# Kernel tuning notes

Hardware: AMD Instinct MI355X
Metric: run time of the kernel (lower is better)

The kernel has to match this reference:

```python
import jax, jax.numpy as jnp
import numpy as np

K = 15          # k_point_level
EPS = 1e-5      # BatchNorm eps
NEG = 0.2       # LeakyReLU slope


def _lrelu(y):
    return jnp.where(y > 0, y, NEG * y)


def _knn_idx(x, k):
    # x: [N, C, P] -> idx [N, P, k] of nearest points (incl. self) by -||xi-xj||^2 topk
    inner = -2.0 * jnp.einsum('ncp,ncq->npq', x, x)
    xx = jnp.sum(x * x, axis=1)                      # [N, P]
    pd = -xx[:, :, None] - inner - xx[:, None, :]    # [N, P, P]
    return jax.lax.top_k(pd, k)[1]


def _edge_feature(x, k):
    # x: [N, C, P] -> [N, P, k, 2C] = concat(neigh - center, center)
    N = x.shape[0]
    idx = _knn_idx(x, k)                             # [N, P, k]
    xt = jnp.transpose(x, (0, 2, 1))                 # [N, P, C]
    neigh = xt[jnp.arange(N)[:, None, None], idx]    # [N, P, k, C]
    center = jnp.broadcast_to(xt[:, :, None, :], neigh.shape)
    return jnp.concatenate([neigh - center, center], axis=-1)


def _edge_block(x, W, gamma, beta, k):
    # EdgeConv: gather -> 1x1 conv -> BN (batch stats) -> LeakyReLU -> max over k
    f = _edge_feature(x, k)                          # [N, P, k, 2C]
    y = jnp.einsum('npkc,oc->npko', f, W)
    m = jnp.mean(y, axis=(0, 1, 2))
    v = jnp.var(y, axis=(0, 1, 2))
    y = (y - m) * jax.lax.rsqrt(v + EPS) * gamma + beta
    y = jnp.max(_lrelu(y), axis=2)                   # [N, P, O]
    return jnp.transpose(y, (0, 2, 1))               # [N, O, P]


def _forward(x, W1, g1, b1, W2, g2, b2, W3, g3, b3, W4, g4, b4,
             W5, g5, b5, Wl1, g6, b6, Wl2, bl2, g7, b7, Wl3, bl3):
    x1 = _edge_block(x, W1, g1, b1, K)               # [N, 64, P]
    x2 = _edge_block(x1, W2, g2, b2, K)              # [N, 64, P]
    x3 = _edge_block(x2, W3, g3, b3, K)              # [N, 128, P]
    x4 = _edge_block(x3, W4, g4, b4, K)              # [N, 256, P]
    xc = jnp.concatenate([x1, x2, x3, x4], axis=1)   # [N, 512, P]
    y = jnp.einsum('ncp,oc->npo', xc, W5)            # [N, P, emb]
    m = jnp.mean(y, axis=(0, 1)); v = jnp.var(y, axis=(0, 1))
    y = _lrelu((y - m) * jax.lax.rsqrt(v + EPS) * g5 + b5)
    h = jnp.concatenate([jnp.max(y, axis=1), jnp.mean(y, axis=1)], axis=1)  # [N, 2*emb]
    h = h @ Wl1.T
    m = jnp.mean(h, axis=0); v = jnp.var(h, axis=0)
    h = _lrelu((h - m) * jax.lax.rsqrt(v + EPS) * g6 + b6)
    h = h @ Wl2.T + bl2
    m = jnp.mean(h, axis=0); v = jnp.var(h, axis=0)
    h = _lrelu((h - m) * jax.lax.rsqrt(v + EPS) * g7 + b7)
    logits = h @ Wl3.T + bl3
    return jax.nn.log_softmax(logits, axis=1)


def setup_inputs() -> dict:
    key = jax.random.key(0)
    ks = iter(jax.random.split(key, 16))
    N, P, EMB, NC = 2048, 32, 1024, 800

    def w(k, o, i):
        return jax.random.normal(k, (o, i), jnp.float32) / np.sqrt(i)

    d = {
        'x': jax.random.normal(next(ks), (N, 3, P), jnp.float32),
        'info_point_set': jnp.zeros((1,), jnp.float32),
        'W1': w(next(ks), 64, 6),   'g1': jnp.ones(64),  'b1': jnp.zeros(64),
        'W2': w(next(ks), 64, 128), 'g2': jnp.ones(64),  'b2': jnp.zeros(64),
        'W3': w(next(ks), 128, 128),'g3': jnp.ones(128), 'b3': jnp.zeros(128),
        'W4': w(next(ks), 256, 256),'g4': jnp.ones(256), 'b4': jnp.zeros(256),
        'W5': w(next(ks), EMB, 512),'g5': jnp.ones(EMB), 'b5': jnp.zeros(EMB),
        'Wl1': w(next(ks), 512, 2 * EMB), 'g6': jnp.ones(512), 'b6': jnp.zeros(512),
        'Wl2': w(next(ks), 256, 512), 'bl2': jnp.zeros(256),
        'g7': jnp.ones(256), 'b7': jnp.zeros(256),
        'Wl3': w(next(ks), NC, 256), 'bl3': jnp.zeros(NC),
    }
    return d


def reference(x, info_point_set, W1, g1, b1, W2, g2, b2, W3, g3, b3,
              W4, g4, b4, W5, g5, b5, Wl1, g6, b6, Wl2, bl2, g7, b7, Wl3, bl3):
    # info_point_set unused: args.k + args.k_global == 0 path (dynamic KNN graph).
    return _forward(x, W1, g1, b1, W2, g2, b2, W3, g3, b3, W4, g4, b4,
                    W5, g5, b5, Wl1, g6, b6, Wl2, bl2, g7, b7, Wl3, bl3)
```

## Files before the change

### kernel.cpp

```cpp
#include <hip/hip_runtime.h>
#include <hip/hip_bf16.h>
#include <cstdint>
#include <cstddef>

#define NPTS 2048
#define P 32
#define KNN_K 15
#define LRELU_NEG 0.2f
#define BN_EPS 1e-5f

__device__ __forceinline__ float lrelu(float x) { return x > 0.f ? x : LRELU_NEG * x; }

__device__ __forceinline__ unsigned short f2bf(float x) {
    union { float f; unsigned u; } uu; uu.f = x;
    unsigned r = uu.u + 0x7fffu + ((uu.u >> 16) & 1u);
    return (unsigned short)(r >> 16);
}
__device__ __forceinline__ float bf2f(unsigned short b) {
    union { unsigned u; float f; } uu; uu.u = ((unsigned)b) << 16;
    return uu.f;
}

typedef short bf16x8 __attribute__((ext_vector_type(8)));
typedef float f32x4  __attribute__((ext_vector_type(4)));

template<int C>
__global__ __launch_bounds__(64) void knn_kernel(const float* __restrict__ xin, int cloudStride,
                                                 unsigned char* __restrict__ idx)
{
    const int n = blockIdx.x, t = threadIdx.x;
    __shared__ float xs[C][P];
    __shared__ float xx[P];
    __shared__ float pd[P][P + 1];
    const float* xp = xin + (size_t)n * cloudStride;
    for (int i = t; i < C * P; i += 64) xs[i / P][i % P] = xp[i];
    __syncthreads();
    if (t < P) { float s = 0.f; for (int c = 0; c < C; ++c) { float v = xs[c][t]; s = fmaf(v, v, s); } xx[t] = s; }
    __syncthreads();
    for (int i = t; i < P * P; i += 64) {
        int p = i >> 5, q = i & 31;
        float d = 0.f;
        for (int c = 0; c < C; ++c) d = fmaf(xs[c][p], xs[c][q], d);
        pd[p][q] = 2.f * d - xx[p] - xx[q];
    }
    __syncthreads();
    if (t < P) {
        for (int j = 0; j < KNN_K; ++j) {
            float best = -INFINITY; int bq = 0;
            for (int q = 0; q < P; ++q) { float v = pd[t][q]; if (v > best) { best = v; bq = q; } }
            idx[(size_t)n * (P * KNN_K) + t * KNN_K + j] = (unsigned char)bq;
            pd[t][bq] = -INFINITY;
        }
    }
}

__global__ __launch_bounds__(256) void build_wcat_kernel(const float* __restrict__ W, float* __restrict__ wt,
                                                         int C, int O, int NCHUNK)
{
    int i = blockIdx.x * 256 + threadIdx.x;
    int tot = C * 2 * O;
    if (i >= tot) return;
    int c = i / (2 * O), col = i % (2 * O);
    int O2C = 2 * O / NCHUNK, OC = O / NCHUNK;
    int chunk = col / O2C, cl = col % O2C;
    float v;
    if (cl < OC) { int o = chunk * OC + cl; v = W[(size_t)o * 2 * C + c]; }
    else { int o = chunk * OC + cl - OC; v = W[(size_t)o * 2 * C + C + c] - W[(size_t)o * 2 * C + c]; }
    wt[i] = v;
}

__global__ __launch_bounds__(256) void pack_wcat_kernel(const float* __restrict__ wt,
                                                        unsigned short* __restrict__ wpk,
                                                        int C, int TOTC)
{
    int NTT = TOTC / 16;
    int total = C * TOTC;
    int i = blockIdx.x * 256 + threadIdx.x;
    if (i >= total) return;
    int j = i & 7, lane = (i >> 3) & 63;
    int rest = i >> 9;
    int ntg = rest % NTT, kb = rest / NTT;
    int k = kb * 32 + (lane >> 4) * 8 + j;
    int col = ntg * 16 + (lane & 15);
    float f = wt[(size_t)k * TOTC + col];
    unsigned short hi = f2bf(f);
    unsigned short lo = f2bf(f - bf2f(hi));
    size_t base = (size_t)rest * 1024 + (size_t)lane * 8 + j;
    wpk[base] = hi;
    wpk[base + 512] = lo;
}

template<int C, int O, int NCHUNK, bool OUT>
__global__ __launch_bounds__(256) void edge_pass_kernel(
    const float* __restrict__ xin, int cloudStride,
    const float* __restrict__ wt,
    const unsigned char* __restrict__ idx,
    const float* __restrict__ st,
    float* __restrict__ xcout,
    float* __restrict__ partS, float* __restrict__ partQ)
{
    constexpr int TOTC = 2 * O;
    constexpr int O2C = TOTC / NCHUNK;
    constexpr int OC  = O / NCHUNK;
    constexpr int TPC = (O2C >= 256) ? 1 : (256 / O2C);
    constexpr int CPT = (O2C > 256) ? (O2C / 256) : 1;
    constexpr int PP  = P / TPC;
    constexpr int TPO = 256 / OC;
    constexpr int PPo = P / TPO;
    const int n = blockIdx.x, t = threadIdx.x;

    __shared__ float xs[C][P];
    __shared__ float gh[P * O2C];
    __shared__ unsigned char idl[P * KNN_K];
    __shared__ float red[2][256];

    const float* xp = xin + (size_t)n * cloudStride;
    for (int i = t; i < C * P; i += 256) xs[i / P][i % P] = xp[i];
    for (int i = t; i < P * KNN_K; i += 256) idl[i] = idx[(size_t)n * (P * KNN_K) + i];

    const int col = (O2C >= 256) ? t : (t % O2C);
    const int p0  = ((O2C >= 256) ? 0 : (t / O2C)) * PP;
    const int o   = t % OC;
    const int p0c = (t / OC) * PPo;

    for (int chunk = 0; chunk < NCHUNK; ++chunk) {
        __syncthreads();
        {
            float acc[CPT][PP];
            #pragma unroll
            for (int j = 0; j < CPT; ++j)
                #pragma unroll
                for (int p = 0; p < PP; ++p) acc[j][p] = 0.f;
            for (int c = 0; c < C; ++c) {
                float w[CPT];
                #pragma unroll
                for (int j = 0; j < CPT; ++j) w[j] = wt[(size_t)c * TOTC + chunk * O2C + col + j * 256];
                #pragma unroll
                for (int p = 0; p < PP; ++p) {
                    float xv = xs[c][p0 + p];
                    #pragma unroll
                    for (int j = 0; j < CPT; ++j) acc[j][p] = fmaf(w[j], xv, acc[j][p]);
                }
            }
            #pragma unroll
            for (int j = 0; j < CPT; ++j)
                #pragma unroll
                for (int p = 0; p < PP; ++p) gh[(p0 + p) * O2C + col + j * 256] = acc[j][p];
        }
        __syncthreads();

        if constexpr (!OUT) {
            float ssum = 0.f, ssq = 0.f;
            #pragma unroll
            for (int p = 0; p < PPo; ++p) {
                const int pp = p0c + p;
                const float g = gh[pp * O2C + OC + o];
                #pragma unroll
                for (int k = 0; k < KNN_K; ++k) {
                    const int q = idl[pp * KNN_K + k];
                    float yv = gh[q * O2C + o] + g;
                    ssum += yv; ssq += yv * yv;
                }
            }
            red[0][t] = ssum; red[1][t] = ssq;
            __syncthreads();
            if (t < OC) {
                float S = 0.f, Q = 0.f;
                #pragma unroll
                for (int j = 0; j < TPO; ++j) { S += red[0][t + j * OC]; Q += red[1][t + j * OC]; }
                partS[(size_t)(chunk * OC + t) * 2048 + n] = S;
                partQ[(size_t)(chunk * OC + t) * 2048 + n] = Q;
            }
        } else {
            const float s = st[chunk * OC + o], sh = st[1024 + chunk * OC + o];
            float rbuf[PPo];
            #pragma unroll
            for (int p = 0; p < PPo; ++p) {
                const int pp = p0c + p;
                const float g = gh[pp * O2C + OC + o];
                float mx = -INFINITY, mn = INFINITY;
                #pragma unroll
                for (int k = 0; k < KNN_K; ++k) {
                    const int q = idl[pp * KNN_K + k];
                    float yv = gh[q * O2C + o] + g;
                    mx = fmaxf(mx, yv); mn = fminf(mn, yv);
                }
                rbuf[p] = lrelu(fmaf(s, (s >= 0.f ? mx : mn), sh));
            }
            __syncthreads();
            #pragma unroll
            for (int p = 0; p < PPo; ++p) gh[o * (P + 1) + p0c + p] = rbuf[p];
            __syncthreads();
            for (int i = t; i < OC * P; i += 256)
                xcout[(size_t)n * (512 * P) + chunk * OC * P + i] = gh[(i / P) * (P + 1) + (i % P)];
        }
    }
}

template<int C, int O, bool OUT>
__global__ __launch_bounds__(256) void edge_mfma_kernel(
    const float* __restrict__ xin, int cloudStride,
    const unsigned short* __restrict__ wpk,
    const unsigned char* __restrict__ idx,
    const float* __restrict__ st,
    float* __restrict__ xcout,
    float* __restrict__ partS, float* __restrict__ partQ)
{
    constexpr int TOTC  = 2 * O;
    constexpr int O2C   = (TOTC > 256) ? 256 : TOTC;
    constexpr int NCHUNK= TOTC / O2C;
    constexpr int OC    = O2C / 2;
    constexpr int NTW   = O2C / 64;
    constexpr int KB    = C / 32;
    constexpr int NTT   = TOTC / 16;
    constexpr int AS    = C + 8;
    constexpr int GHS   = O2C + 4;
    constexpr int TPO   = 256 / OC;
    constexpr int PPo   = P / TPO;

    const int n = blockIdx.x, t = threadIdx.x;
    const int w = t >> 6, l = t & 63;
    const int lg = l >> 4, lm = l & 15;

    __shared__ unsigned short Ah[P * AS];
    __shared__ unsigned short Al[P * AS];
    __shared__ float gh[P * GHS];
    __shared__ unsigned char idl[P * KNN_K];

    const float* xp = xin + (size_t)n * cloudStride;
    for (int i = t; i < C * P; i += 256) {
        int c = i / P, p = i % P;
        float v = xp[i];
        unsigned short hi = f2bf(v);
        Ah[p * AS + c] = hi;
        Al[p * AS + c] = f2bf(v - bf2f(hi));
    }
    for (int i = t; i < P * KNN_K; i += 256) idl[i] = idx[(size_t)n * (P * KNN_K) + i];
    __syncthreads();

    const int o = t % OC;
    const int p0c = (t / OC) * PPo;

    for (int chunk = 0; chunk < NCHUNK; ++chunk) {
        f32x4 acc[2][NTW];
        #pragma unroll
        for (int mt = 0; mt < 2; ++mt)
            #pragma unroll
            for (int nt = 0; nt < NTW; ++nt) acc[mt][nt] = (f32x4)0.f;

        #pragma unroll
        for (int kb = 0; kb < KB; ++kb) {
            bf16x8 a_h[2], a_l[2];
            #pragma unroll
            for (int mt = 0; mt < 2; ++mt) {
                int row = mt * 16 + lm;
                a_h[mt] = *(const bf16x8*)&Ah[row * AS + kb * 32 + lg * 8];
                a_l[mt] = *(const bf16x8*)&Al[row * AS + kb * 32 + lg * 8];
            }
            #pragma unroll
            for (int nt = 0; nt < NTW; ++nt) {
                int ntg = chunk * (O2C / 16) + w * NTW + nt;
                const unsigned short* bp = wpk + (size_t)(kb * NTT + ntg) * 1024 + (size_t)l * 8;
                bf16x8 Bh = *(const bf16x8*)bp;
                bf16x8 Bl = *(const bf16x8*)(bp + 512);
                #pragma unroll
                for (int mt = 0; mt < 2; ++mt) {
                    acc[mt][nt] = __builtin_amdgcn_mfma_f32_16x16x32_bf16(a_h[mt], Bl, acc[mt][nt], 0, 0, 0);
                    acc[mt][nt] = __builtin_amdgcn_mfma_f32_16x16x32_bf16(a_l[mt], Bh, acc[mt][nt], 0, 0, 0);
                    acc[mt][nt] = __builtin_amdgcn_mfma_f32_16x16x32_bf16(a_h[mt], Bh, acc[mt][nt], 0, 0, 0);
                }
            }
        }
        __syncthreads();
        #pragma unroll
        for (int mt = 0; mt < 2; ++mt)
            #pragma unroll
            for (int nt = 0; nt < NTW; ++nt) {
                int colb = (w * NTW + nt) * 16 + lm;
                #pragma unroll
                for (int r = 0; r < 4; ++r)
                    gh[(mt * 16 + lg * 4 + r) * GHS + colb] = acc[mt][nt][r];
            }
        __syncthreads();

        if constexpr (!OUT) {
            float ssum = 0.f, ssq = 0.f;
            #pragma unroll
            for (int p = 0; p < PPo; ++p) {
                const int pp = p0c + p;
                const float g = gh[pp * GHS + OC + o];
                #pragma unroll
                for (int k = 0; k < KNN_K; ++k) {
                    const int q = idl[pp * KNN_K + k];
                    float yv = gh[q * GHS + o] + g;
                    ssum += yv; ssq += yv * yv;
                }
            }
            __syncthreads();
            gh[t] = ssum; gh[256 + t] = ssq;
            __syncthreads();
            if (t < OC) {
                float S = 0.f, Q = 0.f;
                #pragma unroll
                for (int j = 0; j < TPO; ++j) { S += gh[t + j * OC]; Q += gh[256 + t + j * OC]; }
                partS[(size_t)(chunk * OC + t) * 2048 + n] = S;
                partQ[(size_t)(chunk * OC + t) * 2048 + n] = Q;
            }
        } else {
            const float s = st[chunk * OC + o], sh = st[1024 + chunk * OC + o];
            float rbuf[PPo];
            #pragma unroll
            for (int p = 0; p < PPo; ++p) {
                const int pp = p0c + p;
                const float g = gh[pp * GHS + OC + o];
                float mx = -INFINITY, mn = INFINITY;
                #pragma unroll
                for (int k = 0; k < KNN_K; ++k) {
                    const int q = idl[pp * KNN_K + k];
                    float yv = gh[q * GHS + o] + g;
                    mx = fmaxf(mx, yv); mn = fminf(mn, yv);
                }
                rbuf[p] = lrelu(fmaf(s, (s >= 0.f ? mx : mn), sh));
            }
            __syncthreads();
            #pragma unroll
            for (int p = 0; p < PPo; ++p) gh[o * (P + 1) + p0c + p] = rbuf[p];
            __syncthreads();
            for (int i = t; i < OC * P; i += 256)
                xcout[(size_t)n * (512 * P) + chunk * OC * P + i] = gh[(i / P) * (P + 1) + (i % P)];
        }
    }
}

__global__ __launch_bounds__(256) void reduce_stats_kernel(const float* __restrict__ partS,
                                                           const float* __restrict__ partQ,
                                                           const float* __restrict__ gamma,
                                                           const float* __restrict__ beta,
                                                           float* __restrict__ st, int nparts, float inv_count)
{
    const int o = blockIdx.x, t = threadIdx.x;
    __shared__ float rs[256], rq[256];
    float S = 0.f, Q = 0.f;
    for (int i = t; i < nparts; i += 256) { S += partS[(size_t)o * 2048 + i]; Q += partQ[(size_t)o * 2048 + i]; }
    rs[t] = S; rq[t] = Q; __syncthreads();
    for (int w = 128; w > 0; w >>= 1) { if (t < w) { rs[t] += rs[t + w]; rq[t] += rq[t + w]; } __syncthreads(); }
    if (t == 0) {
        float m = rs[0] * inv_count;
        float v = fmaxf(rq[0] * inv_count - m * m, 0.f);
        float s = gamma[o] * rsqrtf(v + BN_EPS);
        st[o] = s;
        st[1024 + o] = fmaf(-m, s, beta[o]);
    }
}

__global__ __launch_bounds__(256) void pack_w5_kernel(const float* __restrict__ W5, unsigned short* __restrict__ wp)
{
    int i = blockIdx.x * 256 + threadIdx.x;
    if (i >= (1 << 19)) return;
    int j = i & 7, lane = (i >> 3) & 63, nt = (i >> 9) & 63, kb = i >> 15;
    int c = kb * 32 + (lane >> 4) * 8 + j;
    int o = nt * 16 + (lane & 15);
    float f = W5[(size_t)o * 512 + c];
    unsigned short hi = f2bf(f);
    unsigned short lo = f2bf(f - bf2f(hi));
    size_t base = (size_t)(kb * 64 + nt) * 2 * 512 + (size_t)lane * 8 + j;
    wp[base] = hi;
    wp[base + 512] = lo;
}

__global__ __launch_bounds__(512) void conv5_store_kernel(
    const float* xc, const unsigned short* __restrict__ wpack,
    unsigned short* y5,
    float* __restrict__ partS, float* __restrict__ partQ)
{
    const int b = blockIdx.x;
    const int t = threadIdx.x;
    const int w = t >> 6, l = t & 63;
    const int lg = l >> 4, lm = l & 15;

    __shared__ unsigned short Ah[2][64][40];
    __shared__ unsigned short Al[2][64][40];

    f32x4 acc[4][8];
    #pragma unroll
    for (int mt = 0; mt < 4; ++mt)
        #pragma unroll
        for (int nt = 0; nt < 8; ++nt) acc[mt][nt] = (f32x4)0.f;

    const float* xbase = xc + (size_t)(b * 2) * (512 * P);

    const int sp4    = t & 7;
    const int schalf = (t >> 3) & 15;
    const int scloud = (t >> 7) & 1;
    const bool sact  = t < 256;

    auto stage = [&](int kb, int buf) {
        if (sact) {
            const float* src = xbase + (size_t)scloud * (512 * P)
                             + (size_t)(kb * 32 + 2 * schalf) * P + sp4 * 4;
            const float4 v0 = *(const float4*)src;
            const float4 v1 = *(const float4*)(src + P);
            const int r0 = scloud * 32 + sp4 * 4;
            #pragma unroll
            for (int e = 0; e < 4; ++e) {
                float a0 = (&v0.x)[e], a1 = (&v1.x)[e];
                unsigned short h0 = f2bf(a0), h1 = f2bf(a1);
                unsigned short l0 = f2bf(a0 - bf2f(h0)), l1 = f2bf(a1 - bf2f(h1));
                *(unsigned*)&Ah[buf][r0 + e][2 * schalf] = (unsigned)h0 | ((unsigned)h1 << 16);
                *(unsigned*)&Al[buf][r0 + e][2 * schalf] = (unsigned)l0 | ((unsigned)l1 << 16);
            }
        }
    };

    stage(0, 0);
    int cur = 0;
    for (int kb = 0; kb < 16; ++kb) {
        __syncthreads();
        if (kb + 1 < 16) stage(kb + 1, cur ^ 1);

        bf16x8 a_h[4], a_l[4];
        #pragma unroll
        for (int mt = 0; mt < 4; ++mt) {
            int row = mt * 16 + lm;
            a_h[mt] = *(const bf16x8*)&Ah[cur][row][lg * 8];
            a_l[mt] = *(const bf16x8*)&Al[cur][row][lg * 8];
        }
        #pragma unroll
        for (int nt = 0; nt < 8; ++nt) {
            const int ntg = w * 8 + nt;
            const unsigned short* bp = wpack + (size_t)(kb * 64 + ntg) * 2 * 512 + (size_t)l * 8;
            bf16x8 Bh = *(const bf16x8*)bp;
            bf16x8 Bl = *(const bf16x8*)(bp + 512);
            #pragma unroll
            for (int mt = 0; mt < 4; ++mt) {
                acc[mt][nt] = __builtin_amdgcn_mfma_f32_16x16x32_bf16(a_h[mt], Bl, acc[mt][nt], 0, 0, 0);
                acc[mt][nt] = __builtin_amdgcn_mfma_f32_16x16x32_bf16(a_l[mt], Bh, acc[mt][nt], 0, 0, 0);
                acc[mt][nt] = __builtin_amdgcn_mfma_f32_16x16x32_bf16(a_h[mt], Bh, acc[mt][nt], 0, 0, 0);
            }
        }
        cur ^= 1;
    }
    __syncthreads();

    #pragma unroll
    for (int nt = 0; nt < 8; ++nt) {
        float s = 0.f, q = 0.f;
        #pragma unroll
        for (int mt = 0; mt < 4; ++mt)
            #pragma unroll
            for (int r = 0; r < 4; ++r) { float v = acc[mt][nt][r]; s += v; q = fmaf(v, v, q); }
        s += __shfl_xor(s, 16); q += __shfl_xor(q, 16);
        s += __shfl_xor(s, 32); q += __shfl_xor(q, 32);
        if (l < 16) {
            int o = w * 128 + nt * 16 + lm;
            partS[(size_t)o * 2048 + b] = s;
            partQ[(size_t)o * 2048 + b] = q;
        }
        #pragma unroll
        for (int mt = 0; mt < 4; ++mt) {
            unsigned p0 = (unsigned)f2bf(acc[mt][nt][0]) | ((unsigned)f2bf(acc[mt][nt][1]) << 16);
            unsigned p1 = (unsigned)f2bf(acc[mt][nt][2]) | ((unsigned)f2bf(acc[mt][nt][3]) << 16);
            size_t off = ((((size_t)b * 8 + w) * 8 + nt) * 4 + mt) * 64 + l;
            ((uint2*)y5)[off] = make_uint2(p0, p1);
        }
    }
}

__global__ __launch_bounds__(512) void conv5_finish_kernel(
    const unsigned short* __restrict__ y5, const float* __restrict__ st, float* __restrict__ h)
{
    const int b = blockIdx.x, t = threadIdx.x;
    const int w = t >> 6, l = t & 63, lm = l & 15;
    #pragma unroll
    for (int nt = 0; nt < 8; ++nt) {
        const int o = w * 128 + nt * 16 + lm;
        const float sc = st[o], sh = st[1024 + o];
        #pragma unroll
        for (int cloud = 0; cloud < 2; ++cloud) {
            float mx = -INFINITY, sm = 0.f;
            #pragma unroll
            for (int half = 0; half < 2; ++half) {
                const int mt = cloud * 2 + half;
                uint2 pk = ((const uint2*)y5)[((((size_t)b * 8 + w) * 8 + nt) * 4 + mt) * 64 + l];
                #pragma unroll
                for (int r = 0; r < 4; ++r) {
                    unsigned word = (r < 2) ? pk.x : pk.y;
                    unsigned short bits = (unsigned short)((r & 1) ? (word >> 16) : (word & 0xffff));
                    float v = lrelu(fmaf(sc, bf2f(bits), sh));
                    mx = fmaxf(mx, v); sm += v;
                }
            }
            mx = fmaxf(mx, __shfl_xor(mx, 16)); sm += __shfl_xor(sm, 16);
            mx = fmaxf(mx, __shfl_xor(mx, 32)); sm += __shfl_xor(sm, 32);
            if (l < 16) {
                const int n = b * 2 + cloud;
                h[(size_t)n * 2048 + o] = mx;
                h[(size_t)n * 2048 + 1024 + o] = sm * (1.f / 32.f);
            }
        }
    }
}

__global__ __launch_bounds__(256) void gemm_nt(const float* __restrict__ A, const float* __restrict__ B,
                                               const float* __restrict__ bias, float* __restrict__ Cc,
                                               int M, int Nn, int Kk)
{
    __shared__ float As[16][64];
    __shared__ float Bs[16][64];
    const int t = threadIdx.x;
    const int m0 = blockIdx.y * 64;
    const int o0 = blockIdx.x * 64;
    const int lm = t % 64;
    const int lk4 = (t / 64) * 4;
    const int tx = t % 16, ty = t / 16;
    float acc[4][4] = {};
    for (int k0 = 0; k0 < Kk; k0 += 16) {
        float4 av4 = *(const float4*)(A + (size_t)(m0 + lm) * Kk + k0 + lk4);
        float4 bv4 = make_float4(0.f, 0.f, 0.f, 0.f);
        if (o0 + lm < Nn) bv4 = *(const float4*)(B + (size_t)(o0 + lm) * Kk + k0 + lk4);
        __syncthreads();
        As[lk4 + 0][lm] = av4.x; As[lk4 + 1][lm] = av4.y; As[lk4 + 2][lm] = av4.z; As[lk4 + 3][lm] = av4.w;
        Bs[lk4 + 0][lm] = bv4.x; Bs[lk4 + 1][lm] = bv4.y; Bs[lk4 + 2][lm] = bv4.z; Bs[lk4 + 3][lm] = bv4.w;
        __syncthreads();
        #pragma unroll
        for (int kk = 0; kk < 16; ++kk) {
            float a[4], b[4];
            *(float4*)a = *(const float4*)&As[kk][ty * 4];
            *(float4*)b = *(const float4*)&Bs[kk][tx * 4];
            #pragma unroll
            for (int i = 0; i < 4; ++i)
                #pragma unroll
                for (int j = 0; j < 4; ++j) acc[i][j] = fmaf(a[i], b[j], acc[i][j]);
        }
    }
    #pragma unroll
    for (int i = 0; i < 4; ++i) {
        int m = m0 + ty * 4 + i;
        #pragma unroll
        for (int j = 0; j < 4; ++j) {
            int o = o0 + tx * 4 + j;
            if (o < Nn) Cc[(size_t)m * Nn + o] = acc[i][j] + (bias ? bias[o] : 0.f);
        }
    }
    (void)M;
}

template<int NCPT>
__global__ __launch_bounds__(256) void colstats_kernel(const float* __restrict__ A, int NC,
                                                       float* __restrict__ partS, float* __restrict__ partQ)
{
    const int b = blockIdx.x, t = threadIdx.x;
    float S[NCPT], Q[NCPT];
    #pragma unroll
    for (int j = 0; j < NCPT; ++j) { S[j] = 0.f; Q[j] = 0.f; }
    for (int r = 0; r < 32; ++r) {
        const float* row = A + (size_t)(b * 32 + r) * NC;
        #pragma unroll
        for (int j = 0; j < NCPT; ++j) { float v = row[t + j * 256]; S[j] += v; Q[j] += v * v; }
    }
    #pragma unroll
    for (int j = 0; j < NCPT; ++j) {
        int o = t + j * 256;
        partS[(size_t)o * 2048 + b] = S[j];
        partQ[(size_t)o * 2048 + b] = Q[j];
    }
}

__global__ __launch_bounds__(256) void bnact_kernel(const float* __restrict__ in, const float* __restrict__ st,
                                                    float* __restrict__ out, int NC, int total)
{
    int i = blockIdx.x * 256 + threadIdx.x;
    if (i < total) {
        int o = i % NC;
        out[i] = lrelu(fmaf(st[o], in[i], st[1024 + o]));
    }
}

__global__ __launch_bounds__(256) void logsoftmax_kernel(float* __restrict__ out)
{
    const int n = blockIdx.x, t = threadIdx.x;
    float* row = out + (size_t)n * 800;
    __shared__ float red[256];
    float v[4];
    float mx = -INFINITY;
    #pragma unroll
    for (int j = 0; j < 4; ++j) {
        int i = t + j * 256;
        v[j] = (i < 800) ? row[i] : -INFINITY;
        mx = fmaxf(mx, v[j]);
    }
    red[t] = mx; __syncthreads();
    for (int w = 128; w > 0; w >>= 1) { if (t < w) red[t] = fmaxf(red[t], red[t + w]); __syncthreads(); }
    const float m = red[0]; __syncthreads();
    float s = 0.f;
    #pragma unroll
    for (int j = 0; j < 4; ++j) { int i = t + j * 256; if (i < 800) s += expf(v[j] - m); }
    red[t] = s; __syncthreads();
    for (int w = 128; w > 0; w >>= 1) { if (t < w) red[t] += red[t + w]; __syncthreads(); }
    const float lg = m + logf(red[0]);
    #pragma unroll
    for (int j = 0; j < 4; ++j) { int i = t + j * 256; if (i < 800) row[i] = v[j] - lg; }
}

extern "C" void kernel_launch(void* const* d_in, const int* in_sizes, int n_in,
                              void* d_out, int out_size, void* d_ws, size_t ws_size,
                              hipStream_t stream)
{
    (void)in_sizes; (void)n_in; (void)out_size; (void)ws_size;
    const float* x   = (const float*)d_in[0];
    const float* W1  = (const float*)d_in[2];
    const float* g1  = (const float*)d_in[3];
    const float* b1  = (const float*)d_in[4];
    const float* W2  = (const float*)d_in[5];
    const float* g2  = (const float*)d_in[6];
    const float* b2  = (const float*)d_in[7];
    const float* W3  = (const float*)d_in[8];
    const float* g3  = (const float*)d_in[9];
    const float* b3  = (const float*)d_in[10];
    const float* W4  = (const float*)d_in[11];
    const float* g4  = (const float*)d_in[12];
    const float* b4  = (const float*)d_in[13];
    const float* W5  = (const float*)d_in[14];
    const float* g5  = (const float*)d_in[15];
    const float* b5  = (const float*)d_in[16];
    const float* Wl1 = (const float*)d_in[17];
    const float* g6  = (const float*)d_in[18];
    const float* b6  = (const float*)d_in[19];
    const float* Wl2 = (const float*)d_in[20];
    const float* bl2 = (const float*)d_in[21];
    const float* g7  = (const float*)d_in[22];
    const float* b7  = (const float*)d_in[23];
    const float* Wl3 = (const float*)d_in[24];
    const float* bl3 = (const float*)d_in[25];

    char* ws = (char*)d_ws;
    size_t off = 0;
    auto alloc = [&](size_t bytes) -> void* {
        void* p = ws + off; off += (bytes + 255) & ~(size_t)255; return p;
    };
    float*          xc    = (float*)alloc((size_t)NPTS * 512 * P * 4);
    unsigned char*  idx   = (unsigned char*)alloc((size_t)NPTS * P * KNN_K);
    float*          partS = (float*)alloc((size_t)1024 * 2048 * 4);
    float*          partQ = (float*)alloc((size_t)1024 * 2048 * 4);
    float*          st    = (float*)alloc(2048 * 4);
    float*          wt    = (float*)alloc((size_t)512 * 1024 * 4);
    unsigned short* wpk   = (unsigned short*)alloc((size_t)128 * 512 * 2 * 2);
    float*          h     = (float*)alloc((size_t)2048 * 2048 * 4);
    float*          h1p   = (float*)alloc((size_t)2048 * 512 * 4);
    unsigned short* y5 = (unsigned short*)xc;
    float* h1  = h;
    float* h2p = h + 1048576;
    float* h2  = h + 1572864;

    const float inv_edge = 1.f / (float)(NPTS * P * KNN_K);

    knn_kernel<3><<<NPTS, 64, 0, stream>>>(x, 3 * P, idx);
    build_wcat_kernel<<<(3 * 128 + 255) / 256, 256, 0, stream>>>(W1, wt, 3, 64, 1);
    edge_pass_kernel<3, 64, 1, false><<<NPTS, 256, 0, stream>>>(x, 3 * P, wt, idx, nullptr, nullptr, partS, partQ);
    reduce_stats_kernel<<<64, 256, 0, stream>>>(partS, partQ, g1, b1, st, 2048, inv_edge);
    edge_pass_kernel<3, 64, 1, true><<<NPTS, 256, 0, stream>>>(x, 3 * P, wt, idx, st, xc + 0 * P, nullptr, nullptr);

    knn_kernel<64><<<NPTS, 64, 0, stream>>>(xc, 512 * P, idx);
    build_wcat_kernel<<<(64 * 128 + 255) / 256, 256, 0, stream>>>(W2, wt, 64, 64, 1);
    pack_wcat_kernel<<<(64 * 128 + 255) / 256, 256, 0, stream>>>(wt, wpk, 64, 128);
    edge_mfma_kernel<64, 64, false><<<NPTS, 256, 0, stream>>>(xc, 512 * P, wpk, idx, nullptr, nullptr, partS, partQ);
    reduce_stats_kernel<<<64, 256, 0, stream>>>(partS, partQ, g2, b2, st, 2048, inv_edge);
    edge_mfma_kernel<64, 64, true><<<NPTS, 256, 0, stream>>>(xc, 512 * P, wpk, idx, st, xc + 64 * P, nullptr, nullptr);

    knn_kernel<64><<<NPTS, 64, 0, stream>>>(xc + 64 * P, 512 * P, idx);
    build_wcat_kernel<<<(64 * 256 + 255) / 256, 256, 0, stream>>>(W3, wt, 64, 128, 1);
    pack_wcat_kernel<<<(64 * 256 + 255) / 256, 256, 0, stream>>>(wt, wpk, 64, 256);
    edge_mfma_kernel<64, 128, false><<<NPTS, 256, 0, stream>>>(xc + 64 * P, 512 * P, wpk, idx, nullptr, nullptr, partS, partQ);
    reduce_stats_kernel<<<128, 256, 0, stream>>>(partS, partQ, g3, b3, st, 2048, inv_edge);
    edge_mfma_kernel<64, 128, true><<<NPTS, 256, 0, stream>>>(xc + 64 * P, 512 * P, wpk, idx, st, xc + 128 * P, nullptr, nullptr);

    knn_kernel<128><<<NPTS, 64, 0, stream>>>(xc + 128 * P, 512 * P, idx);
    build_wcat_kernel<<<(128 * 512 + 255) / 256, 256, 0, stream>>>(W4, wt, 128, 256, 2);
    pack_wcat_kernel<<<(128 * 512 + 255) / 256, 256, 0, stream>>>(wt, wpk, 128, 512);
    edge_mfma_kernel<128, 256, false><<<NPTS, 256, 0, stream>>>(xc + 128 * P, 512 * P, wpk, idx, nullptr, nullptr, partS, partQ);
    reduce_stats_kernel<<<256, 256, 0, stream>>>(partS, partQ, g4, b4, st, 2048, inv_edge);
    edge_mfma_kernel<128, 256, true><<<NPTS, 256, 0, stream>>>(xc + 128 * P, 512 * P, wpk, idx, st, xc + 256 * P, nullptr, nullptr);

    pack_w5_kernel<<<2048, 256, 0, stream>>>(W5, (unsigned short*)wt);
    conv5_store_kernel<<<1024, 512, 0, stream>>>(xc, (const unsigned short*)wt, y5, partS, partQ);
    reduce_stats_kernel<<<1024, 256, 0, stream>>>(partS, partQ, g5, b5, st, 1024, 1.f / 65536.f);
    conv5_finish_kernel<<<1024, 512, 0, stream>>>(y5, st, h);

    gemm_nt<<<dim3(512 / 64, 2048 / 64), 256, 0, stream>>>(h, Wl1, nullptr, h1p, 2048, 512, 2048);
    colstats_kernel<2><<<64, 256, 0, stream>>>(h1p, 512, partS, partQ);
    reduce_stats_kernel<<<512, 256, 0, stream>>>(partS, partQ, g6, b6, st, 64, 1.f / 2048.f);
    bnact_kernel<<<(2048 * 512 + 255) / 256, 256, 0, stream>>>(h1p, st, h1, 512, 2048 * 512);

    gemm_nt<<<dim3(256 / 64, 2048 / 64), 256, 0, stream>>>(h1, Wl2, bl2, h2p, 2048, 256, 512);
    colstats_kernel<1><<<64, 256, 0, stream>>>(h2p, 256, partS, partQ);
    reduce_stats_kernel<<<256, 256, 0, stream>>>(partS, partQ, g7, b7, st, 64, 1.f / 2048.f);
    bnact_kernel<<<(2048 * 256 + 255) / 256, 256, 0, stream>>>(h2p, st, h2, 256, 2048 * 256);

    gemm_nt<<<dim3((800 + 63) / 64, 2048 / 64), 256, 0, stream>>>(h2, Wl3, bl3, (float*)d_out, 2048, 800, 256);
    logsoftmax_kernel<<<NPTS, 256, 0, stream>>>((float*)d_out);
}
```

Measured before the change: 946.7 us.

## Move FC head GEMMs to split-bf16 MFMA with fused BN stats and input activation

Replaces the scalar fp32 tiled GEMM for the three classifier linear layers with an MFMA kernel. It uses a hi/lo bf16 split (three MFMAs per tile) to keep near-fp32 accuracy, with weights pre-packed by a new pack kernel. Column statistics are now accumulated in the GEMM epilogue, and the BN+LeakyReLU of the previous layer is applied while staging the input. This drops the separate colstats and bnact passes. Edge-conv weight packing also merges the build and pack kernels into one. In exchange there are extra bf16 conversion steps, and the split-bf16 arithmetic may differ slightly from plain fp32.

```diff
diff --git a/kernel.cpp b/kernel.cpp
--- a/kernel.cpp
+++ b/kernel.cpp
@@ -69,25 +69,41 @@
     wt[i] = v;
 }
 
-__global__ __launch_bounds__(256) void pack_wcat_kernel(const float* __restrict__ wt,
+__global__ __launch_bounds__(256) void pack_wcat_direct(const float* __restrict__ W,
                                                         unsigned short* __restrict__ wpk,
-                                                        int C, int TOTC)
-{
-    int NTT = TOTC / 16;
-    int total = C * TOTC;
+                                                        int C, int O, int NCHUNK)
+{
+    const int TOTC = 2 * O, NTT = TOTC / 16;
+    const int O2C = TOTC / NCHUNK, OC = O / NCHUNK;
     int i = blockIdx.x * 256 + threadIdx.x;
-    if (i >= total) return;
-    int j = i & 7, lane = (i >> 3) & 63;
-    int rest = i >> 9;
+    if (i >= C * TOTC) return;
+    int j = i & 7, lane = (i >> 3) & 63, rest = i >> 9;
     int ntg = rest % NTT, kb = rest / NTT;
     int k = kb * 32 + (lane >> 4) * 8 + j;
     int col = ntg * 16 + (lane & 15);
-    float f = wt[(size_t)k * TOTC + col];
-    unsigned short hi = f2bf(f);
-    unsigned short lo = f2bf(f - bf2f(hi));
-    size_t base = (size_t)rest * 1024 + (size_t)lane * 8 + j;
-    wpk[base] = hi;
-    wpk[base + 512] = lo;
+    int chunk = col / O2C, cl = col % O2C;
+    float v;
+    if (cl < OC) { int o = chunk * OC + cl; v = W[(size_t)o * 2 * C + k]; }
+    else         { int o = chunk * OC + cl - OC; v = W[(size_t)o * 2 * C + C + k] - W[(size_t)o * 2 * C + k]; }
+    unsigned short hi = f2bf(v);
+    wpk[(size_t)rest * 1024 + lane * 8 + j] = hi;
+    wpk[(size_t)rest * 1024 + 512 + lane * 8 + j] = f2bf(v - bf2f(hi));
+}
+
+__global__ __launch_bounds__(256) void pack_wfc_kernel(const float* __restrict__ W,
+                                                       unsigned short* __restrict__ wpk,
+                                                       int Kk, int Nn, int NTT)
+{
+    int i = blockIdx.x * 256 + threadIdx.x;
+    if (i >= NTT * 16 * Kk) return;
+    int j = i & 7, lane = (i >> 3) & 63, rest = i >> 9;
+    int ntg = rest % NTT, kb = rest / NTT;
+    int k = kb * 32 + (lane >> 4) * 8 + j;
+    int col = ntg * 16 + (lane & 15);
+    float v = (col < Nn) ? W[(size_t)col * Kk + k] : 0.f;
+    unsigned short hi = f2bf(v);
+    wpk[(size_t)rest * 1024 + lane * 8 + j] = hi;
+    wpk[(size_t)rest * 1024 + 512 + lane * 8 + j] = f2bf(v - bf2f(hi));
 }
 
 template<int C, int O, int NCHUNK, bool OUT>
@@ -501,78 +517,102 @@
     }
 }
 
-__global__ __launch_bounds__(256) void gemm_nt(const float* __restrict__ A, const float* __restrict__ B,
-                                               const float* __restrict__ bias, float* __restrict__ Cc,
-                                               int M, int Nn, int Kk)
-{
-    __shared__ float As[16][64];
-    __shared__ float Bs[16][64];
+template<bool BNIN, bool STATS>
+__global__ __launch_bounds__(256) void gemm_mfma_nt(
+    const float* __restrict__ A, const unsigned short* __restrict__ wpk,
+    const float* __restrict__ stbn, const float* __restrict__ bias,
+    float* __restrict__ Cc, float* __restrict__ partS, float* __restrict__ partQ,
+    int Nn, int NTT, int Kk)
+{
+    const int o0 = blockIdx.x * 64;
+    const int m0 = blockIdx.y * 64;
     const int t = threadIdx.x;
-    const int m0 = blockIdx.y * 64;
-    const int o0 = blockIdx.x * 64;
-    const int lm = t % 64;
-    const int lk4 = (t / 64) * 4;
-    const int tx = t % 16, ty = t / 16;
-    float acc[4][4] = {};
-    for (int k0 = 0; k0 < Kk; k0 += 16) {
-        float4 av4 = *(const float4*)(A + (size_t)(m0 + lm) * Kk + k0 + lk4);
-        float4 bv4 = make_float4(0.f, 0.f, 0.f, 0.f);
-        if (o0 + lm < Nn) bv4 = *(const float4*)(B + (size_t)(o0 + lm) * Kk + k0 + lk4);
+    const int w = t >> 6, l = t & 63;
+    const int lg = l >> 4, lm = l & 15;
+
+    __shared__ unsigned short Ah[2][64][40];
+    __shared__ unsigned short Al[2][64][40];
+
+    f32x4 acc[4];
+    #pragma unroll
+    for (int mt = 0; mt < 4; ++mt) acc[mt] = (f32x4)0.f;
+
+    const int srow = t >> 3;
+    const int sk4  = (t & 7) * 4;
+
+    auto stage = [&](int kb, int buf) {
+        const float* src = A + (size_t)(m0 + srow) * Kk + kb * 32 + sk4;
+        float4 v0 = *(const float4*)src;
+        float4 v1 = *(const float4*)(src + (size_t)32 * Kk);
+        if (BNIN) {
+            const float4 s4 = *(const float4*)(stbn + kb * 32 + sk4);
+            const float4 t4 = *(const float4*)(stbn + 1024 + kb * 32 + sk4);
+            #pragma unroll
+            for (int e = 0; e < 4; ++e) {
+                (&v0.x)[e] = lrelu(fmaf((&s4.x)[e], (&v0.x)[e], (&t4.x)[e]));
+                (&v1.x)[e] = lrelu(fmaf((&s4.x)[e], (&v1.x)[e], (&t4.x)[e]));
+            }
+        }
+        #pragma unroll
+        for (int e = 0; e < 4; e += 2) {
+            float a0 = (&v0.x)[e], a1 = (&v0.x)[e + 1];
+            unsigned short h0 = f2bf(a0), h1 = f2bf(a1);
+            *(unsigned*)&Ah[buf][srow][sk4 + e] = (unsigned)h0 | ((unsigned)h1 << 16);
+            *(unsigned*)&Al[buf][srow][sk4 + e] =
+                (unsigned)f2bf(a0 - bf2f(h0)) | ((unsigned)f2bf(a1 - bf2f(h1)) << 16);
+            float b0 = (&v1.x)[e], b1 = (&v1.x)[e + 1];
+            unsigned short g0 = f2bf(b0), g1 = f2bf(b1);
+            *(unsigned*)&Ah[buf][srow + 32][sk4 + e] = (unsigned)g0 | ((unsigned)g1 << 16);
+            *(unsigned*)&Al[buf][srow + 32][sk4 + e] =
+                (unsigned)f2bf(b0 - bf2f(g0)) | ((unsigned)f2bf(b1 - bf2f(g1)) << 16);
+        }
+    };
+
+    const int KB = Kk >> 5;
+    stage(0, 0);
+    int cur = 0;
+    const int ntg = blockIdx.x * 4 + w;
+    for (int kb = 0; kb < KB; ++kb) {
         __syncthreads();
-        As[lk4 + 0][lm] = av4.x; As[lk4 + 1][lm] = av4.y; As[lk4 + 2][lm] = av4.z; As[lk4 + 3][lm] = av4.w;
-        Bs[lk4 + 0][lm] = bv4.x; Bs[lk4 + 1][lm] = bv4.y; Bs[lk4 + 2][lm] = bv4.z; Bs[lk4 + 3][lm] = bv4.w;
-        __syncthreads();
-        #pragma unroll
-        for (int kk = 0; kk < 16; ++kk) {
-            float a[4], b[4];
-            *(float4*)a = *(const float4*)&As[kk][ty * 4];
-            *(float4*)b = *(const float4*)&Bs[kk][tx * 4];
-            #pragma unroll
-            for (int i = 0; i < 4; ++i)
-                #pragma unroll
-                for (int j = 0; j < 4; ++j) acc[i][j] = fmaf(a[i], b[j], acc[i][j]);
-        }
-    }
+        if (kb + 1 < KB) stage(kb + 1, cur ^ 1);
+        bf16x8 a_h[4], a_l[4];
+        #pragma unroll
+        for (int mt = 0; mt < 4; ++mt) {
+            a_h[mt] = *(const bf16x8*)&Ah[cur][mt * 16 + lm][lg * 8];
+            a_l[mt] = *(const bf16x8*)&Al[cur][mt * 16 + lm][lg * 8];
+        }
+        const unsigned short* bp = wpk + ((size_t)kb * NTT + ntg) * 1024 + (size_t)l * 8;
+        bf16x8 Bh = *(const bf16x8*)bp;
+        bf16x8 Bl = *(const bf16x8*)(bp + 512);
+        #pragma unroll
+        for (int mt = 0; mt < 4; ++mt) {
+            acc[mt] = __builtin_amdgcn_mfma_f32_16x16x32_bf16(a_h[mt], Bl, acc[mt], 0, 0, 0);
+            acc[mt] = __builtin_amdgcn_mfma_f32_16x16x32_bf16(a_l[mt], Bh, acc[mt], 0, 0, 0);
+            acc[mt] = __builtin_amdgcn_mfma_f32_16x16x32_bf16(a_h[mt], Bh, acc[mt], 0, 0, 0);
+        }
+        cur ^= 1;
+    }
+
+    const int col = o0 + w * 16 + lm;
+    const bool cok = col < Nn;
+    const float bv = (bias != nullptr && cok) ? bias[col] : 0.f;
+    float s = 0.f, q = 0.f;
     #pragma unroll
-    for (int i = 0; i < 4; ++i) {
-        int m = m0 + ty * 4 + i;
-        #pragma unroll
-        for (int j = 0; j < 4; ++j) {
-            int o = o0 + tx * 4 + j;
-            if (o < Nn) Cc[(size_t)m * Nn + o] = acc[i][j] + (bias ? bias[o] : 0.f);
-        }
-    }
-    (void)M;
-}
-
-template<int NCPT>
-__global__ __launch_bounds__(256) void colstats_kernel(const float* __restrict__ A, int NC,
-                                                       float* __restrict__ partS, float* __restrict__ partQ)
-{
-    const int b = blockIdx.x, t = threadIdx.x;
-    float S[NCPT], Q[NCPT];
-    #pragma unroll
-    for (int j = 0; j < NCPT; ++j) { S[j] = 0.f; Q[j] = 0.f; }
-    for (int r = 0; r < 32; ++r) {
-        const float* row = A + (size_t)(b * 32 + r) * NC;
-        #pragma unroll
-        for (int j = 0; j < NCPT; ++j) { float v = row[t + j * 256]; S[j] += v; Q[j] += v * v; }
-    }
-    #pragma unroll
-    for (int j = 0; j < NCPT; ++j) {
-        int o = t + j * 256;
-        partS[(size_t)o * 2048 + b] = S[j];
-        partQ[(size_t)o * 2048 + b] = Q[j];
-    }
-}
-
-__global__ __launch_bounds__(256) void bnact_kernel(const float* __restrict__ in, const float* __restrict__ st,
-                                                    float* __restrict__ out, int NC, int total)
-{
-    int i = blockIdx.x * 256 + threadIdx.x;
-    if (i < total) {
-        int o = i % NC;
-        out[i] = lrelu(fmaf(st[o], in[i], st[1024 + o]));
+    for (int mt = 0; mt < 4; ++mt) {
+        #pragma unroll
+        for (int r = 0; r < 4; ++r) {
+            float v = acc[mt][r] + bv;
+            if (STATS) { s += v; q = fmaf(v, v, q); }
+            if (cok) Cc[(size_t)(m0 + mt * 16 + lg * 4 + r) * Nn + col] = v;
+        }
+    }
+    if (STATS) {
+        s += __shfl_xor(s, 16); q += __shfl_xor(q, 16);
+        s += __shfl_xor(s, 32); q += __shfl_xor(q, 32);
+        if (l < 16 && cok) {
+            partS[(size_t)col * 2048 + blockIdx.y] = s;
+            partQ[(size_t)col * 2048 + blockIdx.y] = q;
+        }
     }
 }
 
@@ -645,12 +685,11 @@
     float*          st    = (float*)alloc(2048 * 4);
     float*          wt    = (float*)alloc((size_t)512 * 1024 * 4);
     unsigned short* wpk   = (unsigned short*)alloc((size_t)128 * 512 * 2 * 2);
+    unsigned short* fcpk  = (unsigned short*)alloc((size_t)512 * 2048 * 2 * 2);
     float*          h     = (float*)alloc((size_t)2048 * 2048 * 4);
     float*          h1p   = (float*)alloc((size_t)2048 * 512 * 4);
     unsigned short* y5 = (unsigned short*)xc;
-    float* h1  = h;
     float* h2p = h + 1048576;
-    float* h2  = h + 1572864;
 
     const float inv_edge = 1.f / (float)(NPTS * P * KNN_K);
 
@@ -661,22 +700,19 @@
     edge_pass_kernel<3, 64, 1, true><<<NPTS, 256, 0, stream>>>(x, 3 * P, wt, idx, st, xc + 0 * P, nullptr, nullptr);
 
     knn_kernel<64><<<NPTS, 64, 0, stream>>>(xc, 512 * P, idx);
-    build_wcat_kernel<<<(64 * 128 + 255) / 256, 256, 0, stream>>>(W2, wt, 64, 64, 1);
-    pack_wcat_kernel<<<(64 * 128 + 255) / 256, 256, 0, stream>>>(wt, wpk, 64, 128);
+    pack_wcat_direct<<<(64 * 128 + 255) / 256, 256, 0, stream>>>(W2, wpk, 64, 64, 1);
     edge_mfma_kernel<64, 64, false><<<NPTS, 256, 0, stream>>>(xc, 512 * P, wpk, idx, nullptr, nullptr, partS, partQ);
     reduce_stats_kernel<<<64, 256, 0, stream>>>(partS, partQ, g2, b2, st, 2048, inv_edge);
     edge_mfma_kernel<64, 64, true><<<NPTS, 256, 0, stream>>>(xc, 512 * P, wpk, idx, st, xc + 64 * P, nullptr, nullptr);
 
     knn_kernel<64><<<NPTS, 64, 0, stream>>>(xc + 64 * P, 512 * P, idx);
-    build_wcat_kernel<<<(64 * 256 + 255) / 256, 256, 0, stream>>>(W3, wt, 64, 128, 1);
-    pack_wcat_kernel<<<(64 * 256 + 255) / 256, 256, 0, stream>>>(wt, wpk, 64, 256);
+    pack_wcat_direct<<<(64 * 256 + 255) / 256, 256, 0, stream>>>(W3, wpk, 64, 128, 1);
     edge_mfma_kernel<64, 128, false><<<NPTS, 256, 0, stream>>>(xc + 64 * P, 512 * P, wpk, idx, nullptr, nullptr, partS, partQ);
     reduce_stats_kernel<<<128, 256, 0, stream>>>(partS, partQ, g3, b3, st, 2048, inv_edge);
     edge_mfma_kernel<64, 128, true><<<NPTS, 256, 0, stream>>>(xc + 64 * P, 512 * P, wpk, idx, st, xc + 128 * P, nullptr, nullptr);
 
     knn_kernel<128><<<NPTS, 64, 0, stream>>>(xc + 128 * P, 512 * P, idx);
-    build_wcat_kernel<<<(128 * 512 + 255) / 256, 256, 0, stream>>>(W4, wt, 128, 256, 2);
-    pack_wcat_kernel<<<(128 * 512 + 255) / 256, 256, 0, stream>>>(wt, wpk, 128, 512);
+    pack_wcat_direct<<<(128 * 512 + 255) / 256, 256, 0, stream>>>(W4, wpk, 128, 256, 2);
     edge_mfma_kernel<128, 256, false><<<NPTS, 256, 0, stream>>>(xc + 128 * P, 512 * P, wpk, idx, nullptr, nullptr, partS, partQ);
     reduce_stats_kernel<<<256, 256, 0, stream>>>(partS, partQ, g4, b4, st, 2048, inv_edge);
     edge_mfma_kernel<128, 256, true><<<NPTS, 256, 0, stream>>>(xc + 128 * P, 512 * P, wpk, idx, st, xc + 256 * P, nullptr, nullptr);
@@ -686,16 +722,16 @@
     reduce_stats_kernel<<<1024, 256, 0, stream>>>(partS, partQ, g5, b5, st, 1024, 1.f / 65536.f);
     conv5_finish_kernel<<<1024, 512, 0, stream>>>(y5, st, h);
 
-    gemm_nt<<<dim3(512 / 64, 2048 / 64), 256, 0, stream>>>(h, Wl1, nullptr, h1p, 2048, 512, 2048);
-    colstats_kernel<2><<<64, 256, 0, stream>>>(h1p, 512, partS, partQ);
-    reduce_stats_kernel<<<512, 256, 0, stream>>>(partS, partQ, g6, b6, st, 64, 1.f / 2048.f);
-    bnact_kernel<<<(2048 * 512 + 255) / 256, 256, 0, stream>>>(h1p, st, h1, 512, 2048 * 512);
-
-    gemm_nt<<<dim3(256 / 64, 2048 / 64), 256, 0, stream>>>(h1, Wl2, bl2, h2p, 2048, 256, 512);
-    colstats_kernel<1><<<64, 256, 0, stream>>>(h2p, 256, partS, partQ);
-    reduce_stats_kernel<<<256, 256, 0, stream>>>(partS, partQ, g7, b7, st, 64, 1.f / 2048.f);
-    bnact_kernel<<<(2048 * 256 + 255) / 256, 256, 0, stream>>>(h2p, st, h2, 256, 2048 * 256);
-
-    gemm_nt<<<dim3((800 + 63) / 64, 2048 / 64), 256, 0, stream>>>(h2, Wl3, bl3, (float*)d_out, 2048, 800, 256);
+    pack_wfc_kernel<<<4096, 256, 0, stream>>>(Wl1, fcpk, 2048, 512, 32);
+    gemm_mfma_nt<false, true><<<dim3(8, 32), 256, 0, stream>>>(h, fcpk, nullptr, nullptr, h1p, partS, partQ, 512, 32, 2048);
+    reduce_stats_kernel<<<512, 256, 0, stream>>>(partS, partQ, g6, b6, st, 32, 1.f / 2048.f);
+
+    pack_wfc_kernel<<<512, 256, 0, stream>>>(Wl2, fcpk, 512, 256, 16);
+    gemm_mfma_nt<true, true><<<dim3(4, 32), 256, 0, stream>>>(h1p, fcpk, st, bl2, h2p, partS, partQ, 256, 16, 512);
+    reduce_stats_kernel<<<256, 256, 0, stream>>>(partS, partQ, g7, b7, st, 32, 1.f / 2048.f);
+
+    pack_wfc_kernel<<<832, 256, 0, stream>>>(Wl3, fcpk, 256, 800, 52);
+    gemm_mfma_nt<true, false><<<dim3(13, 32), 256, 0, stream>>>(h2p, fcpk, st, bl3, (float*)d_out, nullptr, nullptr, 800, 52, 256);
+
     logsoftmax_kernel<<<NPTS, 256, 0, stream>>>((float*)d_out);
 }
```

Result: faster. 851.1 us (-10.1%).
